# Kernel optimization log

Hardware: AMD Instinct MI355X
Metric: run time of the kernel (lower is better)

The kernel has to match this reference:

```python
import jax, jax.numpy as jnp
import numpy as np

B, L, H, T, C = 64, 1024, 512, 100, 97


def setup_inputs() -> dict:
    key = jax.random.key(0)
    k1, k2, k3, k4, k5 = jax.random.split(key, 5)
    return {
        "position_fmap": jax.random.normal(k1, (B, L, H), dtype=jnp.float32),
        "origin_fmap": jax.random.normal(k2, (B, L, H), dtype=jnp.float32),
        "pos_emb": jax.random.normal(k3, (T, H), dtype=jnp.float32),
        "W_gen": jax.random.normal(k4, (C, H), dtype=jnp.float32) * (1.0 / np.sqrt(H)),
        "b_gen": jax.random.normal(k5, (C,), dtype=jnp.float32) * 0.01,
    }


def reference(position_fmap, origin_fmap, pos_emb, W_gen, b_gen):
    # The torch loop over t in [0, T) computes, per step, scores = fmap @ emb_t,
    # softmax over L, then context = a^T @ origin_fmap. Batched over all steps:
    scores = jnp.einsum('blh,th->btl', position_fmap, pos_emb)   # [B, T, L]
    attn = jax.nn.softmax(scores, axis=-1)                       # softmax over spatial L
    context = jnp.einsum('btl,blh->bth', attn, origin_fmap)      # [B, T, H]
    # generator: Linear(H -> num_classes)
    return jnp.einsum('bth,ch->btc', context, W_gen) + b_gen     # [B, T, C]
```

## Files before the change

kernel.cpp:

```cpp
#include <hip/hip_runtime.h>

#define B_   64
#define L_   1024
#define H_   512
#define T_   100
#define C_   97
#define TP_  112

typedef _Float16 h8 __attribute__((ext_vector_type(8)));
typedef __attribute__((ext_vector_type(4))) float f32x4;

__global__ __launch_bounds__(256) void k0_prep(
    const float* __restrict__ emb, const float* __restrict__ W,
    _Float16* __restrict__ embh, _Float16* __restrict__ Wh) {
  const int row = blockIdx.x, tid = threadIdx.x;
  if (row < TP_) {
    for (int j = tid; j < H_; j += 256)
      embh[(size_t)row * H_ + j] =
          (row < T_) ? (_Float16)emb[(size_t)row * H_ + j] : (_Float16)0.f;
  } else {
    const int c = row - TP_;
    for (int j = tid; j < H_; j += 256)
      Wh[(size_t)c * H_ + j] =
          (c < C_) ? (_Float16)W[(size_t)c * H_ + j] : (_Float16)0.f;
  }
}

__global__ __launch_bounds__(256) void k1_scores(
    const float* __restrict__ fmap, const _Float16* __restrict__ embh,
    _Float16* __restrict__ sc, float* __restrict__ part) {
  __shared__ float red_m[4 * TP_];
  __shared__ float red_s[4 * TP_];
  __shared__ float sMb[TP_];
  const int tid = threadIdx.x;
  const int wave = tid >> 6, lane = tid & 63;
  const int quad = lane >> 4, cc = lane & 15;
  const int m0 = blockIdx.x * 64 + wave * 16;

  f32x4 acc[7];
#pragma unroll
  for (int i = 0; i < 7; ++i) acc[i] = (f32x4){0.f, 0.f, 0.f, 0.f};

  const float* ap = fmap + (size_t)(m0 + cc) * H_ + quad * 8;
#pragma unroll 2
  for (int k = 0; k < H_; k += 32) {
    float4 x0 = *(const float4*)(ap + k);
    float4 x1 = *(const float4*)(ap + k + 4);
    h8 a;
    a[0] = (_Float16)x0.x; a[1] = (_Float16)x0.y;
    a[2] = (_Float16)x0.z; a[3] = (_Float16)x0.w;
    a[4] = (_Float16)x1.x; a[5] = (_Float16)x1.y;
    a[6] = (_Float16)x1.z; a[7] = (_Float16)x1.w;
#pragma unroll
    for (int i = 0; i < 7; ++i) {
      h8 bf = *(const h8*)(embh + (size_t)(i * 16 + cc) * H_ + k + quad * 8);
      acc[i] = __builtin_amdgcn_mfma_f32_16x16x32_f16(a, bf, acc[i], 0, 0, 0);
    }
  }

  float pm[7], ps[7];
#pragma unroll
  for (int i = 0; i < 7; ++i) {
    float m = fmaxf(fmaxf(acc[i][0], acc[i][1]), fmaxf(acc[i][2], acc[i][3]));
    float s = 0.f;
#pragma unroll
    for (int r = 0; r < 4; ++r) s += __expf(acc[i][r] - m);
    pm[i] = m; ps[i] = s;
  }
#pragma unroll
  for (int d = 16; d < 64; d <<= 1) {
#pragma unroll
    for (int i = 0; i < 7; ++i) {
      float om = __shfl_xor(pm[i], d, 64);
      float os = __shfl_xor(ps[i], d, 64);
      float M = fmaxf(pm[i], om);
      ps[i] = ps[i] * __expf(pm[i] - M) + os * __expf(om - M);
      pm[i] = M;
    }
  }
  if (lane < 16) {
#pragma unroll
    for (int i = 0; i < 7; ++i) {
      red_m[wave * TP_ + i * 16 + lane] = pm[i];
      red_s[wave * TP_ + i * 16 + lane] = ps[i];
    }
  }
  __syncthreads();
  if (tid < TP_) {
    float M = red_m[tid], S = red_s[tid];
#pragma unroll
    for (int w = 1; w < 4; ++w) {
      float om = red_m[w * TP_ + tid], os = red_s[w * TP_ + tid];
      float nM = fmaxf(M, om);
      S = S * __expf(M - nM) + os * __expf(om - nM);
      M = nM;
    }
    float* p = part + ((size_t)blockIdx.x * TP_ + tid) * 2;
    p[0] = M; p[1] = S;
    sMb[tid] = M;
  }
  __syncthreads();
#pragma unroll
  for (int i = 0; i < 7; ++i) {
    float mb = sMb[i * 16 + cc];
#pragma unroll
    for (int r = 0; r < 4; ++r)
      sc[(size_t)(m0 + quad * 4 + r) * TP_ + i * 16 + cc] =
          (_Float16)(acc[i][r] - mb);
  }
}

__global__ __launch_bounds__(256) void k2_gmat(
    const float* __restrict__ origin, const _Float16* __restrict__ Wh,
    _Float16* __restrict__ G) {
  const int tid = threadIdx.x;
  const int wave = tid >> 6, lane = tid & 63;
  const int quad = lane >> 4, cc = lane & 15;
  const int m0 = blockIdx.x * 64 + wave * 16;

  f32x4 acc[7];
#pragma unroll
  for (int i = 0; i < 7; ++i) acc[i] = (f32x4){0.f, 0.f, 0.f, 0.f};

  const float* ap = origin + (size_t)(m0 + cc) * H_ + quad * 8;
#pragma unroll 2
  for (int k = 0; k < H_; k += 32) {
    float4 x0 = *(const float4*)(ap + k);
    float4 x1 = *(const float4*)(ap + k + 4);
    h8 a;
    a[0] = (_Float16)x0.x; a[1] = (_Float16)x0.y;
    a[2] = (_Float16)x0.z; a[3] = (_Float16)x0.w;
    a[4] = (_Float16)x1.x; a[5] = (_Float16)x1.y;
    a[6] = (_Float16)x1.z; a[7] = (_Float16)x1.w;
#pragma unroll
    for (int i = 0; i < 7; ++i) {
      h8 bf = *(const h8*)(Wh + (size_t)(i * 16 + cc) * H_ + k + quad * 8);
      acc[i] = __builtin_amdgcn_mfma_f32_16x16x32_f16(a, bf, acc[i], 0, 0, 0);
    }
  }
#pragma unroll
  for (int i = 0; i < 7; ++i)
#pragma unroll
    for (int r = 0; r < 4; ++r)
      G[(size_t)(m0 + quad * 4 + r) * TP_ + i * 16 + cc] =
          (_Float16)acc[i][r];
}

__global__ __launch_bounds__(512) void k3_fused(
    const _Float16* __restrict__ sc, const _Float16* __restrict__ G,
    const float* __restrict__ part, const float* __restrict__ bias,
    float* __restrict__ out) {
  __shared__ float sAdj[16][16];
  __shared__ float sInv[16];
  __shared__ f32x4 sred[8][4][64];
  const int bid = blockIdx.x;
  const int b = bid / 14;
  const int rem = bid % 14;
  const int mt = rem >> 1;
  const int ng = rem & 1;
  const int NT = ng ? 3 : 4;
  const int ncol0 = ng * 64;
  const int tid = threadIdx.x;
  const int w = tid >> 6, lane = tid & 63;
  const int quad = lane >> 4, cc = lane & 15;

  if (tid < 16) {
    const int t = mt * 16 + tid;
    float mM[16];
    float M = -1e30f, S = 0.f;
#pragma unroll
    for (int s = 0; s < 16; ++s) {
      const float* p = part + ((size_t)(b * 16 + s) * TP_ + t) * 2;
      float om = p[0], os = p[1];
      mM[s] = om;
      float nM = fmaxf(M, om);
      S = S * __expf(M - nM) + os * __expf(om - nM);
      M = nM;
    }
    sInv[tid] = 1.f / S;
#pragma unroll
    for (int s = 0; s < 16; ++s) sAdj[s][tid] = mM[s] - M;
  }
  __syncthreads();

  f32x4 acc[4];
#pragma unroll
  for (int i = 0; i < 4; ++i) acc[i] = (f32x4){0.f, 0.f, 0.f, 0.f};

  const float inv = sInv[cc];
  const _Float16* scp = sc + (size_t)b * L_ * TP_ + mt * 16 + cc;
  const _Float16* gp  = G  + (size_t)b * L_ * TP_ + ncol0 + cc;
  const int kbase = w * 128;
#pragma unroll 2
  for (int l0 = kbase; l0 < kbase + 128; l0 += 32) {
    const int r0 = l0 + quad * 8;
    const float adj = sAdj[r0 >> 6][cc];
    h8 a;
#pragma unroll
    for (int j = 0; j < 8; ++j) {
      float sv = (float)scp[(size_t)(r0 + j) * TP_];
      a[j] = (_Float16)(__expf(sv + adj) * inv);
    }
#pragma unroll
    for (int nt = 0; nt < 4; ++nt) {
      if (nt < NT) {
        h8 bf;
#pragma unroll
        for (int j = 0; j < 8; ++j)
          bf[j] = gp[(size_t)(r0 + j) * TP_ + nt * 16];
        acc[nt] = __builtin_amdgcn_mfma_f32_16x16x32_f16(a, bf, acc[nt], 0, 0, 0);
      }
    }
  }

#pragma unroll
  for (int nt = 0; nt < 4; ++nt)
    if (nt < NT) sred[w][nt][lane] = acc[nt];
  __syncthreads();

  if (w < NT) {
    f32x4 s = sred[0][w][lane];
#pragma unroll
    for (int ww = 1; ww < 8; ++ww) s += sred[ww][w][lane];
    const int c = ncol0 + w * 16 + cc;
    if (c < C_) {
      const float bv = bias[c];
#pragma unroll
      for (int r = 0; r < 4; ++r) {
        const int t = mt * 16 + quad * 4 + r;
        if (t < T_) out[((size_t)b * T_ + t) * C_ + c] = s[r] + bv;
      }
    }
  }
}

extern "C" void kernel_launch(void* const* d_in, const int* in_sizes, int n_in,
                              void* d_out, int out_size, void* d_ws, size_t ws_size,
                              hipStream_t stream) {
  const float* fmap   = (const float*)d_in[0];
  const float* origin = (const float*)d_in[1];
  const float* emb    = (const float*)d_in[2];
  const float* W      = (const float*)d_in[3];
  const float* bias   = (const float*)d_in[4];
  float* out = (float*)d_out;

  char* ws = (char*)d_ws;
  _Float16* embh = (_Float16*)(ws);
  _Float16* Wh   = (_Float16*)(ws + 114688);
  _Float16* sc   = (_Float16*)(ws + 229376);
  float*    part = (float*)   (ws + 14909440);
  _Float16* G    = (_Float16*)(ws + 15826944);

  hipLaunchKernelGGL(k0_prep,   dim3(224),  dim3(256), 0, stream, emb, W, embh, Wh);
  hipLaunchKernelGGL(k1_scores, dim3(1024), dim3(256), 0, stream, fmap, embh, sc, part);
  hipLaunchKernelGGL(k2_gmat,   dim3(1024), dim3(256), 0, stream, origin, Wh, G);
  hipLaunchKernelGGL(k3_fused,  dim3(896),  dim3(512), 0, stream, sc, G, part, bias, out);
}
```

Before: 381.9 us.

## Fuse score and G GEMMs, transpose intermediates to L-contiguous layout

```diff
diff --git a/kernel.cpp b/kernel.cpp
--- a/kernel.cpp
+++ b/kernel.cpp
@@ -12,85 +12,96 @@
 
 __global__ __launch_bounds__(256) void k0_prep(
     const float* __restrict__ emb, const float* __restrict__ W,
-    _Float16* __restrict__ embh, _Float16* __restrict__ Wh) {
+    _Float16* __restrict__ e2, _Float16* __restrict__ w2) {
   const int row = blockIdx.x, tid = threadIdx.x;
   if (row < TP_) {
-    for (int j = tid; j < H_; j += 256)
-      embh[(size_t)row * H_ + j] =
-          (row < T_) ? (_Float16)emb[(size_t)row * H_ + j] : (_Float16)0.f;
+    for (int j = tid; j < H_; j += 256) {
+      float v = (row < T_) ? emb[(size_t)row * H_ + j] : 0.f;
+      e2[((size_t)(j >> 3) * TP_ + row) * 8 + (j & 7)] = (_Float16)v;
+    }
   } else {
     const int c = row - TP_;
-    for (int j = tid; j < H_; j += 256)
-      Wh[(size_t)c * H_ + j] =
-          (c < C_) ? (_Float16)W[(size_t)c * H_ + j] : (_Float16)0.f;
-  }
-}
-
-__global__ __launch_bounds__(256) void k1_scores(
-    const float* __restrict__ fmap, const _Float16* __restrict__ embh,
-    _Float16* __restrict__ sc, float* __restrict__ part) {
-  __shared__ float red_m[4 * TP_];
-  __shared__ float red_s[4 * TP_];
+    for (int j = tid; j < H_; j += 256) {
+      float v = (c < C_) ? W[(size_t)c * H_ + j] : 0.f;
+      w2[((size_t)(j >> 3) * TP_ + c) * 8 + (j & 7)] = (_Float16)v;
+    }
+  }
+}
+
+__global__ __launch_bounds__(256, 4) void k12_fused(
+    const float* __restrict__ fmap, const float* __restrict__ origin,
+    const _Float16* __restrict__ e2, const _Float16* __restrict__ w2,
+    _Float16* __restrict__ scT, _Float16* __restrict__ GT,
+    float* __restrict__ part) {
+  __shared__ float red_m[4][TP_];
+  __shared__ float red_s[4][TP_];
   __shared__ float sMb[TP_];
   const int tid = threadIdx.x;
   const int wave = tid >> 6, lane = tid & 63;
   const int quad = lane >> 4, cc = lane & 15;
-  const int m0 = blockIdx.x * 64 + wave * 16;
-
-  f32x4 acc[7];
-#pragma unroll
-  for (int i = 0; i < 7; ++i) acc[i] = (f32x4){0.f, 0.f, 0.f, 0.f};
-
-  const float* ap = fmap + (size_t)(m0 + cc) * H_ + quad * 8;
+  const int b = blockIdx.x >> 4;
+  const int lb = (blockIdx.x & 15) * 64 + wave * 16 + cc;
+
+  f32x4 accS[7], accG[7];
+#pragma unroll
+  for (int i = 0; i < 7; ++i) {
+    accS[i] = (f32x4){0.f, 0.f, 0.f, 0.f};
+    accG[i] = (f32x4){0.f, 0.f, 0.f, 0.f};
+  }
+
+  const float* fp = fmap   + ((size_t)b * L_ + lb) * H_ + quad * 8;
+  const float* op = origin + ((size_t)b * L_ + lb) * H_ + quad * 8;
+  const _Float16* ep = e2 + (size_t)(quad * TP_ + cc) * 8;
+  const _Float16* wp = w2 + (size_t)(quad * TP_ + cc) * 8;
+
 #pragma unroll 2
   for (int k = 0; k < H_; k += 32) {
-    float4 x0 = *(const float4*)(ap + k);
-    float4 x1 = *(const float4*)(ap + k + 4);
-    h8 a;
-    a[0] = (_Float16)x0.x; a[1] = (_Float16)x0.y;
-    a[2] = (_Float16)x0.z; a[3] = (_Float16)x0.w;
-    a[4] = (_Float16)x1.x; a[5] = (_Float16)x1.y;
-    a[6] = (_Float16)x1.z; a[7] = (_Float16)x1.w;
+    float4 x0 = *(const float4*)(fp + k);
+    float4 x1 = *(const float4*)(fp + k + 4);
+    float4 y0 = *(const float4*)(op + k);
+    float4 y1 = *(const float4*)(op + k + 4);
+    const _Float16* ek = ep + (size_t)(k >> 3) * (TP_ * 8);
+    const _Float16* wk = wp + (size_t)(k >> 3) * (TP_ * 8);
+    h8 bf, bo;
+    bf[0] = (_Float16)x0.x; bf[1] = (_Float16)x0.y;
+    bf[2] = (_Float16)x0.z; bf[3] = (_Float16)x0.w;
+    bf[4] = (_Float16)x1.x; bf[5] = (_Float16)x1.y;
+    bf[6] = (_Float16)x1.z; bf[7] = (_Float16)x1.w;
+    bo[0] = (_Float16)y0.x; bo[1] = (_Float16)y0.y;
+    bo[2] = (_Float16)y0.z; bo[3] = (_Float16)y0.w;
+    bo[4] = (_Float16)y1.x; bo[5] = (_Float16)y1.y;
+    bo[6] = (_Float16)y1.z; bo[7] = (_Float16)y1.w;
 #pragma unroll
     for (int i = 0; i < 7; ++i) {
-      h8 bf = *(const h8*)(embh + (size_t)(i * 16 + cc) * H_ + k + quad * 8);
-      acc[i] = __builtin_amdgcn_mfma_f32_16x16x32_f16(a, bf, acc[i], 0, 0, 0);
-    }
-  }
-
-  float pm[7], ps[7];
+      h8 ae = *(const h8*)(ek + i * 128);
+      accS[i] = __builtin_amdgcn_mfma_f32_16x16x32_f16(ae, bf, accS[i], 0, 0, 0);
+      h8 aw = *(const h8*)(wk + i * 128);
+      accG[i] = __builtin_amdgcn_mfma_f32_16x16x32_f16(aw, bo, accG[i], 0, 0, 0);
+    }
+  }
+
 #pragma unroll
   for (int i = 0; i < 7; ++i) {
-    float m = fmaxf(fmaxf(acc[i][0], acc[i][1]), fmaxf(acc[i][2], acc[i][3]));
-    float s = 0.f;
-#pragma unroll
-    for (int r = 0; r < 4; ++r) s += __expf(acc[i][r] - m);
-    pm[i] = m; ps[i] = s;
-  }
-#pragma unroll
-  for (int d = 16; d < 64; d <<= 1) {
-#pragma unroll
-    for (int i = 0; i < 7; ++i) {
-      float om = __shfl_xor(pm[i], d, 64);
-      float os = __shfl_xor(ps[i], d, 64);
-      float M = fmaxf(pm[i], om);
-      ps[i] = ps[i] * __expf(pm[i] - M) + os * __expf(om - M);
-      pm[i] = M;
-    }
-  }
-  if (lane < 16) {
-#pragma unroll
-    for (int i = 0; i < 7; ++i) {
-      red_m[wave * TP_ + i * 16 + lane] = pm[i];
-      red_s[wave * TP_ + i * 16 + lane] = ps[i];
+#pragma unroll
+    for (int r = 0; r < 4; ++r) {
+      float m = accS[i][r];
+#pragma unroll
+      for (int d = 1; d < 16; d <<= 1) m = fmaxf(m, __shfl_xor(m, d, 64));
+      float e = __expf(accS[i][r] - m);
+#pragma unroll
+      for (int d = 1; d < 16; d <<= 1) e += __shfl_xor(e, d, 64);
+      if (cc == 0) {
+        red_m[wave][i * 16 + quad * 4 + r] = m;
+        red_s[wave][i * 16 + quad * 4 + r] = e;
+      }
     }
   }
   __syncthreads();
   if (tid < TP_) {
-    float M = red_m[tid], S = red_s[tid];
+    float M = red_m[0][tid], S = red_s[0][tid];
 #pragma unroll
     for (int w = 1; w < 4; ++w) {
-      float om = red_m[w * TP_ + tid], os = red_s[w * TP_ + tid];
+      float om = red_m[w][tid], os = red_s[w][tid];
       float nM = fmaxf(M, om);
       S = S * __expf(M - nM) + os * __expf(om - nM);
       M = nM;
@@ -100,54 +111,22 @@
     sMb[tid] = M;
   }
   __syncthreads();
+
+  _Float16* sp = scT + (size_t)b * TP_ * L_ + lb;
+  _Float16* gp = GT  + (size_t)b * TP_ * L_ + lb;
 #pragma unroll
   for (int i = 0; i < 7; ++i) {
-    float mb = sMb[i * 16 + cc];
-#pragma unroll
-    for (int r = 0; r < 4; ++r)
-      sc[(size_t)(m0 + quad * 4 + r) * TP_ + i * 16 + cc] =
-          (_Float16)(acc[i][r] - mb);
-  }
-}
-
-__global__ __launch_bounds__(256) void k2_gmat(
-    const float* __restrict__ origin, const _Float16* __restrict__ Wh,
-    _Float16* __restrict__ G) {
-  const int tid = threadIdx.x;
-  const int wave = tid >> 6, lane = tid & 63;
-  const int quad = lane >> 4, cc = lane & 15;
-  const int m0 = blockIdx.x * 64 + wave * 16;
-
-  f32x4 acc[7];
-#pragma unroll
-  for (int i = 0; i < 7; ++i) acc[i] = (f32x4){0.f, 0.f, 0.f, 0.f};
-
-  const float* ap = origin + (size_t)(m0 + cc) * H_ + quad * 8;
-#pragma unroll 2
-  for (int k = 0; k < H_; k += 32) {
-    float4 x0 = *(const float4*)(ap + k);
-    float4 x1 = *(const float4*)(ap + k + 4);
-    h8 a;
-    a[0] = (_Float16)x0.x; a[1] = (_Float16)x0.y;
-    a[2] = (_Float16)x0.z; a[3] = (_Float16)x0.w;
-    a[4] = (_Float16)x1.x; a[5] = (_Float16)x1.y;
-    a[6] = (_Float16)x1.z; a[7] = (_Float16)x1.w;
-#pragma unroll
-    for (int i = 0; i < 7; ++i) {
-      h8 bf = *(const h8*)(Wh + (size_t)(i * 16 + cc) * H_ + k + quad * 8);
-      acc[i] = __builtin_amdgcn_mfma_f32_16x16x32_f16(a, bf, acc[i], 0, 0, 0);
-    }
-  }
-#pragma unroll
-  for (int i = 0; i < 7; ++i)
-#pragma unroll
-    for (int r = 0; r < 4; ++r)
-      G[(size_t)(m0 + quad * 4 + r) * TP_ + i * 16 + cc] =
-          (_Float16)acc[i][r];
-}
-
-__global__ __launch_bounds__(512) void k3_fused(
-    const _Float16* __restrict__ sc, const _Float16* __restrict__ G,
+#pragma unroll
+    for (int r = 0; r < 4; ++r) {
+      const int t = i * 16 + quad * 4 + r;
+      sp[(size_t)t * L_] = (_Float16)(accS[i][r] - sMb[t]);
+      gp[(size_t)t * L_] = (_Float16)accG[i][r];
+    }
+  }
+}
+
+__global__ __launch_bounds__(512) void k3_out(
+    const _Float16* __restrict__ scT, const _Float16* __restrict__ GT,
     const float* __restrict__ part, const float* __restrict__ bias,
     float* __restrict__ out) {
   __shared__ float sAdj[16][16];
@@ -188,26 +167,21 @@
   for (int i = 0; i < 4; ++i) acc[i] = (f32x4){0.f, 0.f, 0.f, 0.f};
 
   const float inv = sInv[cc];
-  const _Float16* scp = sc + (size_t)b * L_ * TP_ + mt * 16 + cc;
-  const _Float16* gp  = G  + (size_t)b * L_ * TP_ + ncol0 + cc;
+  const _Float16* ap = scT + ((size_t)(b * TP_ + mt * 16 + cc)) * L_ + quad * 8;
+  const _Float16* gp = GT  + ((size_t)(b * TP_ + ncol0 + cc)) * L_ + quad * 8;
   const int kbase = w * 128;
-#pragma unroll 2
+#pragma unroll
   for (int l0 = kbase; l0 < kbase + 128; l0 += 32) {
-    const int r0 = l0 + quad * 8;
-    const float adj = sAdj[r0 >> 6][cc];
+    const float adj = sAdj[(l0 + quad * 8) >> 6][cc];
+    h8 v = *(const h8*)(ap + l0);
     h8 a;
 #pragma unroll
-    for (int j = 0; j < 8; ++j) {
-      float sv = (float)scp[(size_t)(r0 + j) * TP_];
-      a[j] = (_Float16)(__expf(sv + adj) * inv);
-    }
+    for (int j = 0; j < 8; ++j)
+      a[j] = (_Float16)(__expf((float)v[j] + adj) * inv);
 #pragma unroll
     for (int nt = 0; nt < 4; ++nt) {
       if (nt < NT) {
-        h8 bf;
-#pragma unroll
-        for (int j = 0; j < 8; ++j)
-          bf[j] = gp[(size_t)(r0 + j) * TP_ + nt * 16];
+        h8 bf = *(const h8*)(gp + (size_t)(nt * 16) * L_ + l0);
         acc[nt] = __builtin_amdgcn_mfma_f32_16x16x32_f16(a, bf, acc[nt], 0, 0, 0);
       }
     }
@@ -245,14 +219,15 @@
   float* out = (float*)d_out;
 
   char* ws = (char*)d_ws;
-  _Float16* embh = (_Float16*)(ws);
-  _Float16* Wh   = (_Float16*)(ws + 114688);
-  _Float16* sc   = (_Float16*)(ws + 229376);
+  _Float16* e2   = (_Float16*)(ws);
+  _Float16* w2   = (_Float16*)(ws + 114688);
+  _Float16* scT  = (_Float16*)(ws + 229376);
   float*    part = (float*)   (ws + 14909440);
-  _Float16* G    = (_Float16*)(ws + 15826944);
-
-  hipLaunchKernelGGL(k0_prep,   dim3(224),  dim3(256), 0, stream, emb, W, embh, Wh);
-  hipLaunchKernelGGL(k1_scores, dim3(1024), dim3(256), 0, stream, fmap, embh, sc, part);
-  hipLaunchKernelGGL(k2_gmat,   dim3(1024), dim3(256), 0, stream, origin, Wh, G);
-  hipLaunchKernelGGL(k3_fused,  dim3(896),  dim3(512), 0, stream, sc, G, part, bias, out);
-}
+  _Float16* GT   = (_Float16*)(ws + 15826944);
+
+  hipLaunchKernelGGL(k0_prep,   dim3(224),  dim3(256), 0, stream, emb, W, e2, w2);
+  hipLaunchKernelGGL(k12_fused, dim3(1024), dim3(256), 0, stream,
+                     fmap, origin, e2, w2, scT, GT, part);
+  hipLaunchKernelGGL(k3_out,    dim3(896),  dim3(512), 0, stream,
+                     scT, GT, part, bias, out);
+}
```

Measured after the change: 357.7 us. -6.3%, faster.
